# Performance work log

Measured on AMD Instinct MI355X. Metric: run time of the kernel, lower is better.

Reference implementation:

```python
import jax, jax.numpy as jnp
import numpy as np

B, N, E, F_IN, F_OUT = 4, 50000, 800000, 128, 128


def setup_inputs() -> dict:
    key = jax.random.key(0)
    k1, k2, k3, k4, k5 = jax.random.split(key, 5)
    x = jax.random.normal(k1, (B, N, F_IN), dtype=jnp.float32)
    # nn.Linear(in, out, bias=False) weight: [out_features, in_features]
    W = jax.random.normal(k2, (F_OUT, F_IN), dtype=jnp.float32) * (1.0 / np.sqrt(F_IN))
    edge_row = jax.random.randint(k3, (E,), 0, N, dtype=jnp.int64)
    edge_col = jax.random.randint(k4, (E,), 0, N, dtype=jnp.int64)
    edge_vals = jax.random.uniform(k5, (E,), dtype=jnp.float32)
    return {"x": x, "W": W, "edge_row": edge_row, "edge_col": edge_col, "edge_vals": edge_vals}


def reference(x, W, edge_row, edge_col, edge_vals):
    # x: [B, N, F_in]; linear projection (no bias): h = x @ W^T -> [B, N, F_out]
    h = jnp.einsum('bnf,of->bno', x, W)

    # SpMM: out[r] = sum_{edges (r,c)} A[r,c] * h[c], vmapped over batch
    def spmm(hb):  # hb: [N, F_out]
        msg = hb[edge_col] * edge_vals[:, None]  # [E, F_out]
        return jax.ops.segment_sum(msg, edge_row, num_segments=N)

    return jax.vmap(spmm)(h)  # [B, N, F_out]
```

## Files before the change

### kernel.cpp

```cpp
#include <hip/hip_runtime.h>
#include <stdint.h>

#define NB 4
#define NN 50000
#define NE 800000
#define NF 128

#define NBLK 49
#define LDW 136

typedef __attribute__((ext_vector_type(8))) short  bfrag;
typedef __attribute__((ext_vector_type(4))) float  ffrag;
typedef __attribute__((ext_vector_type(4))) short  short4v;
typedef __attribute__((ext_vector_type(4))) float  f32x4;

__device__ inline unsigned short f2bf(float f) {
    unsigned int u = __builtin_bit_cast(unsigned int, f);
    u += 0x7fffu + ((u >> 16) & 1u);
    return (unsigned short)(u >> 16);
}
__device__ inline float bflo(unsigned int u) { return __builtin_bit_cast(float, u << 16); }
__device__ inline float bfhi(unsigned int u) { return __builtin_bit_cast(float, u & 0xffff0000u); }

__global__ __launch_bounds__(256) void gemm_kernel(
    const float* __restrict__ x,
    const float* __restrict__ W,
    unsigned short* __restrict__ h,
    const int* __restrict__ erow,
    int* __restrict__ cnt,
    int M)
{
    __shared__ short wsh[128 * LDW];

    const int tid = threadIdx.x;

    for (int e = blockIdx.x * 256 + tid; e < NE; e += gridDim.x * 256)
        atomicAdd(&cnt[erow[e]], 1);

#pragma unroll
    for (int it = 0; it < 16; ++it) {
        int idx = it * 256 + tid;
        int r   = idx >> 5;
        int c4  = idx & 31;
        float4 wv = *(const float4*)(W + (size_t)r * NF + c4 * 4);
        short4v wsv;
        wsv[0] = (short)f2bf(wv.x); wsv[1] = (short)f2bf(wv.y);
        wsv[2] = (short)f2bf(wv.z); wsv[3] = (short)f2bf(wv.w);
        *(short4v*)&wsh[r * LDW + c4 * 4] = wsv;
    }
    __syncthreads();

    const int w    = tid >> 6;
    const int lane = tid & 63;
    const int q    = lane >> 4;
    const int l15  = lane & 15;
    const int r0   = blockIdx.x * 128 + w * 32;

    const float* xp[2];
#pragma unroll
    for (int i = 0; i < 2; ++i) {
        int gr = r0 + i * 16 + l15;
        gr = gr < M ? gr : M - 1;
        xp[i] = x + (size_t)gr * NF + q * 8;
    }

    ffrag acc[2][8];
#pragma unroll
    for (int i = 0; i < 2; ++i)
#pragma unroll
        for (int j = 0; j < 8; ++j) acc[i][j] = (ffrag)0.f;

#pragma unroll 2
    for (int kc = 0; kc < 4; ++kc) {
        bfrag a[2];
#pragma unroll
        for (int i = 0; i < 2; ++i) {
            float4 u0 = *(const float4*)(xp[i] + kc * 32);
            float4 u1 = *(const float4*)(xp[i] + kc * 32 + 4);
            bfrag t;
            t[0] = (short)f2bf(u0.x); t[1] = (short)f2bf(u0.y);
            t[2] = (short)f2bf(u0.z); t[3] = (short)f2bf(u0.w);
            t[4] = (short)f2bf(u1.x); t[5] = (short)f2bf(u1.y);
            t[6] = (short)f2bf(u1.z); t[7] = (short)f2bf(u1.w);
            a[i] = t;
        }
#pragma unroll
        for (int j = 0; j < 8; ++j) {
            bfrag b = *(const bfrag*)&wsh[(j * 16 + l15) * LDW + kc * 32 + q * 8];
            acc[0][j] = __builtin_amdgcn_mfma_f32_16x16x32_bf16(
                a[0], b, acc[0][j], 0, 0, 0);
            acc[1][j] = __builtin_amdgcn_mfma_f32_16x16x32_bf16(
                a[1], b, acc[1][j], 0, 0, 0);
        }
    }

    __syncthreads();
    short* tile = wsh;
#pragma unroll
    for (int i = 0; i < 2; ++i)
#pragma unroll
        for (int reg = 0; reg < 4; ++reg) {
            int row = w * 32 + i * 16 + q * 4 + reg;
#pragma unroll
            for (int j = 0; j < 8; ++j)
                tile[row * LDW + j * 16 + l15] = (short)f2bf(acc[i][j][reg]);
        }
    __syncthreads();
#pragma unroll
    for (int it = 0; it < 8; ++it) {
        int row = it * 16 + (tid >> 4);
        int m   = blockIdx.x * 128 + row;
        if (m < M) {
            int n  = m % NN;
            int bb = m / NN;
            uint4 v = *(const uint4*)&tile[row * LDW + (tid & 15) * 8];
            *(uint4*)(h + ((size_t)n * NB + bb) * NF + (tid & 15) * 8) = v;
        }
    }
}

__global__ __launch_bounds__(1024) void scan1_kernel(
    const int* __restrict__ cnt, int* __restrict__ rs, int* __restrict__ bsum)
{
    __shared__ int wsum[16];
    const int tid  = threadIdx.x;
    const int lane = tid & 63;
    const int wid  = tid >> 6;
    const int i    = blockIdx.x * 1024 + tid;

    int v = (i < NN) ? cnt[i] : 0;
    int incl = v;
#pragma unroll
    for (int off = 1; off < 64; off <<= 1) {
        int t = __shfl_up(incl, off, 64);
        if (lane >= off) incl += t;
    }
    if (lane == 63) wsum[wid] = incl;
    __syncthreads();
    int woff = 0;
    for (int ww = 0; ww < wid; ++ww) woff += wsum[ww];
    if (i < NN) rs[i] = woff + incl - v;
    if (tid == 0) {
        int tot = 0;
        for (int ww = 0; ww < 16; ++ww) tot += wsum[ww];
        bsum[blockIdx.x] = tot;
    }
}

__global__ void scan2_kernel(int* __restrict__ bsum)
{
    int lane = threadIdx.x;
    int v = (lane < NBLK) ? bsum[lane] : 0;
    int incl = v;
#pragma unroll
    for (int off = 1; off < 64; off <<= 1) {
        int t = __shfl_up(incl, off, 64);
        if (lane >= off) incl += t;
    }
    if (lane < NBLK) bsum[lane] = incl - v;
}

__global__ void scatter_kernel(const int* __restrict__ row,
                               const int* __restrict__ col,
                               const float* __restrict__ val,
                               const int* __restrict__ rs,
                               const int* __restrict__ bsum,
                               int* __restrict__ cursor,
                               uint2* __restrict__ cv_s)
{
    int e = blockIdx.x * 256 + threadIdx.x;
    if (e < NE) {
        int r   = row[e];
        int p   = atomicAdd(&cursor[r], 1);
        int dst = rs[r] + bsum[r >> 10] + p;
        uint2 cv;
        cv.x = (unsigned)col[e];
        cv.y = __builtin_bit_cast(unsigned, val[e]);
        cv_s[dst] = cv;
    }
}

__global__ __launch_bounds__(256) void spmm_kernel(
    const unsigned short* __restrict__ h,
    const int* __restrict__ rs,
    const int* __restrict__ bsum,
    const uint2* __restrict__ cv_s,
    float* __restrict__ out)
{
    const int w    = threadIdx.x >> 6;
    const int lane = threadIdx.x & 63;
    int r = blockIdx.x * 4 + w;
    if (r >= NN) return;
    r = __builtin_amdgcn_readfirstlane(r);

    const int s = rs[r] + bsum[r >> 10];
    const int e = (r + 1 == NN) ? NE : rs[r + 1] + bsum[(r + 1) >> 10];
    const int b    = lane >> 4;
    const int loff = b * NF + (lane & 15) * 8;

    float acc[8];
#pragma unroll
    for (int k = 0; k < 8; ++k) acc[k] = 0.f;

    for (int base = s; base < e; base += 64) {
        const int n = min(64, e - base);
        unsigned long long cvp = 0ull;
        if (lane < n)
            cvp = __builtin_nontemporal_load(
                      (const unsigned long long*)(cv_s + base + lane));
        const int cvx = (int)(unsigned)(cvp & 0xffffffffull);
        const int cvy = (int)(unsigned)(cvp >> 32);

        const int n4 = (n + 3) & ~3;
        for (int i = 0; i < n4; i += 4) {
            const unsigned c0 = (unsigned)__builtin_amdgcn_readlane(cvx, i);
            const unsigned c1 = (unsigned)__builtin_amdgcn_readlane(cvx, i + 1);
            const unsigned c2 = (unsigned)__builtin_amdgcn_readlane(cvx, i + 2);
            const unsigned c3 = (unsigned)__builtin_amdgcn_readlane(cvx, i + 3);
            const uint4 q0 = *(const uint4*)(h + (size_t)c0 * (NB * NF) + loff);
            const uint4 q1 = *(const uint4*)(h + (size_t)c1 * (NB * NF) + loff);
            const uint4 q2 = *(const uint4*)(h + (size_t)c2 * (NB * NF) + loff);
            const uint4 q3 = *(const uint4*)(h + (size_t)c3 * (NB * NF) + loff);
            const float v0 = __builtin_bit_cast(
                float, __builtin_amdgcn_readlane(cvy, i));
            const float v1 = __builtin_bit_cast(
                float, __builtin_amdgcn_readlane(cvy, i + 1));
            const float v2 = __builtin_bit_cast(
                float, __builtin_amdgcn_readlane(cvy, i + 2));
            const float v3 = __builtin_bit_cast(
                float, __builtin_amdgcn_readlane(cvy, i + 3));

            acc[0] += v0 * bflo(q0.x); acc[1] += v0 * bfhi(q0.x);
            acc[2] += v0 * bflo(q0.y); acc[3] += v0 * bfhi(q0.y);
            acc[4] += v0 * bflo(q0.z); acc[5] += v0 * bfhi(q0.z);
            acc[6] += v0 * bflo(q0.w); acc[7] += v0 * bfhi(q0.w);
            acc[0] += v1 * bflo(q1.x); acc[1] += v1 * bfhi(q1.x);
            acc[2] += v1 * bflo(q1.y); acc[3] += v1 * bfhi(q1.y);
            acc[4] += v1 * bflo(q1.z); acc[5] += v1 * bfhi(q1.z);
            acc[6] += v1 * bflo(q1.w); acc[7] += v1 * bfhi(q1.w);
            acc[0] += v2 * bflo(q2.x); acc[1] += v2 * bfhi(q2.x);
            acc[2] += v2 * bflo(q2.y); acc[3] += v2 * bfhi(q2.y);
            acc[4] += v2 * bflo(q2.z); acc[5] += v2 * bfhi(q2.z);
            acc[6] += v2 * bflo(q2.w); acc[7] += v2 * bfhi(q2.w);
            acc[0] += v3 * bflo(q3.x); acc[1] += v3 * bfhi(q3.x);
            acc[2] += v3 * bflo(q3.y); acc[3] += v3 * bfhi(q3.y);
            acc[4] += v3 * bflo(q3.z); acc[5] += v3 * bfhi(q3.z);
            acc[6] += v3 * bflo(q3.w); acc[7] += v3 * bfhi(q3.w);
        }
    }

    float* op = out + ((size_t)b * NN + r) * NF + (lane & 15) * 8;
    *(float4*)op       = make_float4(acc[0], acc[1], acc[2], acc[3]);
    *(float4*)(op + 4) = make_float4(acc[4], acc[5], acc[6], acc[7]);
}

extern "C" void kernel_launch(void* const* d_in, const int* in_sizes, int n_in,
                              void* d_out, int out_size, void* d_ws, size_t ws_size,
                              hipStream_t stream)
{
    const float* x    = (const float*)d_in[0];
    const float* W    = (const float*)d_in[1];
    const int*   erow = (const int*)d_in[2];
    const int*   ecol = (const int*)d_in[3];
    const float* ev   = (const float*)d_in[4];
    float*       out  = (float*)d_out;

    char*  ws  = (char*)d_ws;
    size_t off = 0;
    auto alloc = [&](size_t bytes) -> void* {
        void* p = ws + off;
        off += (bytes + 255) & ~(size_t)255;
        return p;
    };
    unsigned short* h = (unsigned short*)alloc((size_t)NN * NB * NF * sizeof(unsigned short));
    int*   rs     = (int*)  alloc((size_t)(NN + 1) * sizeof(int));
    int*   cnt    = (int*)  alloc((size_t)2 * NN * sizeof(int));
    int*   cursor = cnt + NN;
    int*   bsum   = (int*)  alloc((size_t)64 * sizeof(int));
    uint2* cv_s   = (uint2*)alloc((size_t)NE * sizeof(uint2));

    hipMemsetAsync(cnt, 0, (size_t)2 * NN * sizeof(int), stream);

    const int M = NB * NN;
    gemm_kernel<<<(M + 127) / 128, 256, 0, stream>>>(x, W, h, erow, cnt, M);

    scan1_kernel<<<NBLK, 1024, 0, stream>>>(cnt, rs, bsum);
    scan2_kernel<<<1, 64, 0, stream>>>(bsum);
    scatter_kernel<<<(NE + 255) / 256, 256, 0, stream>>>(erow, ecol, ev, rs,
                                                         bsum, cursor, cv_s);

    spmm_kernel<<<(NN + 3) / 4, 256, 0, stream>>>(h, rs, bsum, cv_s, out);
}
```

Measured before the change: 378.5 us.

## Merge two-level scan into one block, reuse counts as cursor, unroll gather by 8

Replaces the two-kernel block scan with a single 1024-thread block where each thread scans a chunk of 49 counts serially. The row-start array is now absolute, which drops the bsum indirection from scatter and spmm. Scatter decrements the count array in place instead of using a separate cursor, so the memset only clears half as much. The spmm gather loop is unrolled to 8 outstanding 16-byte loads per iteration to raise memory-level parallelism, at the cost of more registers and padded work on short rows. The single-block scan has strided, uncoalesced per-thread reads and runs on one CU.

Measured after the change: 463.6 us. +22.5%, slower.

```diff
diff --git a/kernel.cpp b/kernel.cpp
--- a/kernel.cpp
+++ b/kernel.cpp
@@ -6,13 +6,13 @@
 #define NE 800000
 #define NF 128
 
-#define NBLK 49
+#define SCHUNK 49
 #define LDW 136
 
 typedef __attribute__((ext_vector_type(8))) short  bfrag;
 typedef __attribute__((ext_vector_type(4))) float  ffrag;
 typedef __attribute__((ext_vector_type(4))) short  short4v;
-typedef __attribute__((ext_vector_type(4))) float  f32x4;
+typedef __attribute__((ext_vector_type(4))) unsigned int u32x4;
 
 __device__ inline unsigned short f2bf(float f) {
     unsigned int u = __builtin_bit_cast(unsigned int, f);
@@ -119,60 +119,51 @@
     }
 }
 
-__global__ __launch_bounds__(1024) void scan1_kernel(
-    const int* __restrict__ cnt, int* __restrict__ rs, int* __restrict__ bsum)
-{
-    __shared__ int wsum[16];
+__global__ __launch_bounds__(1024) void scan_kernel(
+    const int* __restrict__ cnt, int* __restrict__ rs)
+{
+    __shared__ int woffs[16];
     const int tid  = threadIdx.x;
     const int lane = tid & 63;
     const int wid  = tid >> 6;
-    const int i    = blockIdx.x * 1024 + tid;
-
-    int v = (i < NN) ? cnt[i] : 0;
-    int incl = v;
+    const int i0   = tid * SCHUNK;
+
+    int sum = 0;
+    for (int j = 0; j < SCHUNK; ++j) {
+        int i = i0 + j;
+        sum += (i < NN) ? cnt[i] : 0;
+    }
+    int incl = sum;
 #pragma unroll
     for (int off = 1; off < 64; off <<= 1) {
         int t = __shfl_up(incl, off, 64);
         if (lane >= off) incl += t;
     }
-    if (lane == 63) wsum[wid] = incl;
+    if (lane == 63) woffs[wid] = incl;
     __syncthreads();
     int woff = 0;
-    for (int ww = 0; ww < wid; ++ww) woff += wsum[ww];
-    if (i < NN) rs[i] = woff + incl - v;
-    if (tid == 0) {
-        int tot = 0;
-        for (int ww = 0; ww < 16; ++ww) tot += wsum[ww];
-        bsum[blockIdx.x] = tot;
-    }
-}
-
-__global__ void scan2_kernel(int* __restrict__ bsum)
-{
-    int lane = threadIdx.x;
-    int v = (lane < NBLK) ? bsum[lane] : 0;
-    int incl = v;
-#pragma unroll
-    for (int off = 1; off < 64; off <<= 1) {
-        int t = __shfl_up(incl, off, 64);
-        if (lane >= off) incl += t;
-    }
-    if (lane < NBLK) bsum[lane] = incl - v;
+    for (int ww = 0; ww < wid; ++ww) woff += woffs[ww];
+    int run = woff + incl - sum;
+
+    for (int j = 0; j < SCHUNK; ++j) {
+        int i = i0 + j;
+        if (i < NN) { rs[i] = run; run += cnt[i]; }
+    }
+    if (tid == 0) rs[NN] = NE;
 }
 
 __global__ void scatter_kernel(const int* __restrict__ row,
                                const int* __restrict__ col,
                                const float* __restrict__ val,
                                const int* __restrict__ rs,
-                               const int* __restrict__ bsum,
-                               int* __restrict__ cursor,
+                               int* __restrict__ cnt,
                                uint2* __restrict__ cv_s)
 {
     int e = blockIdx.x * 256 + threadIdx.x;
     if (e < NE) {
         int r   = row[e];
-        int p   = atomicAdd(&cursor[r], 1);
-        int dst = rs[r] + bsum[r >> 10] + p;
+        int p   = atomicSub(&cnt[r], 1) - 1;
+        int dst = rs[r] + p;
         uint2 cv;
         cv.x = (unsigned)col[e];
         cv.y = __builtin_bit_cast(unsigned, val[e]);
@@ -183,7 +174,6 @@
 __global__ __launch_bounds__(256) void spmm_kernel(
     const unsigned short* __restrict__ h,
     const int* __restrict__ rs,
-    const int* __restrict__ bsum,
     const uint2* __restrict__ cv_s,
     float* __restrict__ out)
 {
@@ -193,8 +183,8 @@
     if (r >= NN) return;
     r = __builtin_amdgcn_readfirstlane(r);
 
-    const int s = rs[r] + bsum[r >> 10];
-    const int e = (r + 1 == NN) ? NE : rs[r + 1] + bsum[(r + 1) >> 10];
+    const int s = rs[r];
+    const int e = rs[r + 1];
     const int b    = lane >> 4;
     const int loff = b * NF + (lane & 15) * 8;
 
@@ -211,41 +201,25 @@
         const int cvx = (int)(unsigned)(cvp & 0xffffffffull);
         const int cvy = (int)(unsigned)(cvp >> 32);
 
-        const int n4 = (n + 3) & ~3;
-        for (int i = 0; i < n4; i += 4) {
-            const unsigned c0 = (unsigned)__builtin_amdgcn_readlane(cvx, i);
-            const unsigned c1 = (unsigned)__builtin_amdgcn_readlane(cvx, i + 1);
-            const unsigned c2 = (unsigned)__builtin_amdgcn_readlane(cvx, i + 2);
-            const unsigned c3 = (unsigned)__builtin_amdgcn_readlane(cvx, i + 3);
-            const uint4 q0 = *(const uint4*)(h + (size_t)c0 * (NB * NF) + loff);
-            const uint4 q1 = *(const uint4*)(h + (size_t)c1 * (NB * NF) + loff);
-            const uint4 q2 = *(const uint4*)(h + (size_t)c2 * (NB * NF) + loff);
-            const uint4 q3 = *(const uint4*)(h + (size_t)c3 * (NB * NF) + loff);
-            const float v0 = __builtin_bit_cast(
-                float, __builtin_amdgcn_readlane(cvy, i));
-            const float v1 = __builtin_bit_cast(
-                float, __builtin_amdgcn_readlane(cvy, i + 1));
-            const float v2 = __builtin_bit_cast(
-                float, __builtin_amdgcn_readlane(cvy, i + 2));
-            const float v3 = __builtin_bit_cast(
-                float, __builtin_amdgcn_readlane(cvy, i + 3));
-
-            acc[0] += v0 * bflo(q0.x); acc[1] += v0 * bfhi(q0.x);
-            acc[2] += v0 * bflo(q0.y); acc[3] += v0 * bfhi(q0.y);
-            acc[4] += v0 * bflo(q0.z); acc[5] += v0 * bfhi(q0.z);
-            acc[6] += v0 * bflo(q0.w); acc[7] += v0 * bfhi(q0.w);
-            acc[0] += v1 * bflo(q1.x); acc[1] += v1 * bfhi(q1.x);
-            acc[2] += v1 * bflo(q1.y); acc[3] += v1 * bfhi(q1.y);
-            acc[4] += v1 * bflo(q1.z); acc[5] += v1 * bfhi(q1.z);
-            acc[6] += v1 * bflo(q1.w); acc[7] += v1 * bfhi(q1.w);
-            acc[0] += v2 * bflo(q2.x); acc[1] += v2 * bfhi(q2.x);
-            acc[2] += v2 * bflo(q2.y); acc[3] += v2 * bfhi(q2.y);
-            acc[4] += v2 * bflo(q2.z); acc[5] += v2 * bfhi(q2.z);
-            acc[6] += v2 * bflo(q2.w); acc[7] += v2 * bfhi(q2.w);
-            acc[0] += v3 * bflo(q3.x); acc[1] += v3 * bfhi(q3.x);
-            acc[2] += v3 * bflo(q3.y); acc[3] += v3 * bfhi(q3.y);
-            acc[4] += v3 * bflo(q3.z); acc[5] += v3 * bfhi(q3.z);
-            acc[6] += v3 * bflo(q3.w); acc[7] += v3 * bfhi(q3.w);
+        const int n8 = (n + 7) & ~7;
+        for (int i = 0; i < n8; i += 8) {
+            unsigned c[8];
+            u32x4 q[8];
+#pragma unroll
+            for (int k = 0; k < 8; ++k)
+                c[k] = (unsigned)__builtin_amdgcn_readlane(cvx, i + k);
+#pragma unroll
+            for (int k = 0; k < 8; ++k)
+                q[k] = *(const u32x4*)(h + (size_t)c[k] * (NB * NF) + loff);
+#pragma unroll
+            for (int k = 0; k < 8; ++k) {
+                const float v = __builtin_bit_cast(
+                    float, __builtin_amdgcn_readlane(cvy, i + k));
+                acc[0] += v * bflo(q[k][0]); acc[1] += v * bfhi(q[k][0]);
+                acc[2] += v * bflo(q[k][1]); acc[3] += v * bfhi(q[k][1]);
+                acc[4] += v * bflo(q[k][2]); acc[5] += v * bfhi(q[k][2]);
+                acc[6] += v * bflo(q[k][3]); acc[7] += v * bfhi(q[k][3]);
+            }
         }
     }
 
@@ -273,21 +247,18 @@
         return p;
     };
     unsigned short* h = (unsigned short*)alloc((size_t)NN * NB * NF * sizeof(unsigned short));
-    int*   rs     = (int*)  alloc((size_t)(NN + 1) * sizeof(int));
-    int*   cnt    = (int*)  alloc((size_t)2 * NN * sizeof(int));
-    int*   cursor = cnt + NN;
-    int*   bsum   = (int*)  alloc((size_t)64 * sizeof(int));
-    uint2* cv_s   = (uint2*)alloc((size_t)NE * sizeof(uint2));
-
-    hipMemsetAsync(cnt, 0, (size_t)2 * NN * sizeof(int), stream);
+    int*   rs   = (int*)  alloc((size_t)(NN + 1) * sizeof(int));
+    int*   cnt  = (int*)  alloc((size_t)NN * sizeof(int));
+    uint2* cv_s = (uint2*)alloc((size_t)NE * sizeof(uint2));
+
+    hipMemsetAsync(cnt, 0, (size_t)NN * sizeof(int), stream);
 
     const int M = NB * NN;
     gemm_kernel<<<(M + 127) / 128, 256, 0, stream>>>(x, W, h, erow, cnt, M);
 
-    scan1_kernel<<<NBLK, 1024, 0, stream>>>(cnt, rs, bsum);
-    scan2_kernel<<<1, 64, 0, stream>>>(bsum);
+    scan_kernel<<<1, 1024, 0, stream>>>(cnt, rs);
     scatter_kernel<<<(NE + 255) / 256, 256, 0, stream>>>(erow, ecol, ev, rs,
-                                                         bsum, cursor, cv_s);
-
-    spmm_kernel<<<(NN + 3) / 4, 256, 0, stream>>>(h, rs, bsum, cv_s, out);
-}
+                                                         cnt, cv_s);
+
+    spmm_kernel<<<(NN + 3) / 4, 256, 0, stream>>>(h, rs, cv_s, out);
+}
```

## Fuse gemm, scan and scatter into one cooperative persistent kernel

Applied to the files above, without the earlier changes.

Replaces the memset, gemm, two scan kernels and scatter with a single cooperative launch of 512 persistent blocks that use grid.sync between phases. The cnt array is now reused as the scatter cursor by decrementing it, which drops the separate cursor buffer and its memset. The scan uses 256-wide blocks with a two-level prefix. The point is to remove several kernel launches and their gaps. In exchange the GEMM runs as a grid-stride persistent loop that restages W for every tile, and grid-wide barriers add their own cost. A non-cooperative fallback path is kept.

New measurement: 593.8 us. +56.9%, slower.

```diff
diff --git a/kernel.cpp b/kernel.cpp
--- a/kernel.cpp
+++ b/kernel.cpp
@@ -1,18 +1,24 @@
 #include <hip/hip_runtime.h>
+#include <hip/hip_cooperative_groups.h>
 #include <stdint.h>
+
+namespace cg = cooperative_groups;
 
 #define NB 4
 #define NN 50000
 #define NE 800000
 #define NF 128
 
-#define NBLK 49
-#define LDW 136
+#define GRID  512
+#define NTHR  256
+#define GSTR  (GRID * NTHR)
+#define NTILE 1563
+#define NSBLK 196
+#define LDW   136
 
 typedef __attribute__((ext_vector_type(8))) short  bfrag;
 typedef __attribute__((ext_vector_type(4))) float  ffrag;
 typedef __attribute__((ext_vector_type(4))) short  short4v;
-typedef __attribute__((ext_vector_type(4))) float  f32x4;
 
 __device__ inline unsigned short f2bf(float f) {
     unsigned int u = __builtin_bit_cast(unsigned int, f);
@@ -22,21 +28,82 @@
 __device__ inline float bflo(unsigned int u) { return __builtin_bit_cast(float, u << 16); }
 __device__ inline float bfhi(unsigned int u) { return __builtin_bit_cast(float, u & 0xffff0000u); }
 
-__global__ __launch_bounds__(256) void gemm_kernel(
-    const float* __restrict__ x,
-    const float* __restrict__ W,
-    unsigned short* __restrict__ h,
-    const int* __restrict__ erow,
-    int* __restrict__ cnt,
-    int M)
-{
-    __shared__ short wsh[128 * LDW];
-
-    const int tid = threadIdx.x;
-
-    for (int e = blockIdx.x * 256 + tid; e < NE; e += gridDim.x * 256)
-        atomicAdd(&cnt[erow[e]], 1);
-
+__device__ __forceinline__ void gemm_tile(
+    const float* __restrict__ x, unsigned short* __restrict__ h,
+    short* wsh, int t, int M, int tid)
+{
+    const int w    = tid >> 6;
+    const int lane = tid & 63;
+    const int q    = lane >> 4;
+    const int l15  = lane & 15;
+    const int r0   = t * 128 + w * 32;
+
+    const float* xp[2];
+#pragma unroll
+    for (int i = 0; i < 2; ++i) {
+        int gr = r0 + i * 16 + l15;
+        gr = gr < M ? gr : M - 1;
+        xp[i] = x + (size_t)gr * NF + q * 8;
+    }
+
+    ffrag acc[2][8];
+#pragma unroll
+    for (int i = 0; i < 2; ++i)
+#pragma unroll
+        for (int j = 0; j < 8; ++j) acc[i][j] = (ffrag)0.f;
+
+#pragma unroll 2
+    for (int kc = 0; kc < 4; ++kc) {
+        bfrag a[2];
+#pragma unroll
+        for (int i = 0; i < 2; ++i) {
+            float4 u0 = *(const float4*)(xp[i] + kc * 32);
+            float4 u1 = *(const float4*)(xp[i] + kc * 32 + 4);
+            bfrag tt;
+            tt[0] = (short)f2bf(u0.x); tt[1] = (short)f2bf(u0.y);
+            tt[2] = (short)f2bf(u0.z); tt[3] = (short)f2bf(u0.w);
+            tt[4] = (short)f2bf(u1.x); tt[5] = (short)f2bf(u1.y);
+            tt[6] = (short)f2bf(u1.z); tt[7] = (short)f2bf(u1.w);
+            a[i] = tt;
+        }
+#pragma unroll
+        for (int j = 0; j < 8; ++j) {
+            bfrag b = *(const bfrag*)&wsh[(j * 16 + l15) * LDW + kc * 32 + q * 8];
+            acc[0][j] = __builtin_amdgcn_mfma_f32_16x16x32_bf16(
+                a[0], b, acc[0][j], 0, 0, 0);
+            acc[1][j] = __builtin_amdgcn_mfma_f32_16x16x32_bf16(
+                a[1], b, acc[1][j], 0, 0, 0);
+        }
+    }
+
+    __syncthreads();
+    short* tile = wsh;
+#pragma unroll
+    for (int i = 0; i < 2; ++i)
+#pragma unroll
+        for (int reg = 0; reg < 4; ++reg) {
+            int row = w * 32 + i * 16 + q * 4 + reg;
+#pragma unroll
+            for (int j = 0; j < 8; ++j)
+                tile[row * LDW + j * 16 + l15] = (short)f2bf(acc[i][j][reg]);
+        }
+    __syncthreads();
+#pragma unroll
+    for (int it = 0; it < 8; ++it) {
+        int row = it * 16 + (tid >> 4);
+        int m   = t * 128 + row;
+        if (m < M) {
+            int n  = m % NN;
+            int bb = m / NN;
+            uint4 v = *(const uint4*)&tile[row * LDW + (tid & 15) * 8];
+            *(uint4*)(h + ((size_t)n * NB + bb) * NF + (tid & 15) * 8) = v;
+        }
+    }
+}
+
+__device__ __forceinline__ void stage_W(const float* __restrict__ W,
+                                        short* wsh, int tid)
+{
 #pragma unroll
     for (int it = 0; it < 16; ++it) {
         int idx = it * 256 + tid;
@@ -48,86 +115,111 @@
         wsv[2] = (short)f2bf(wv.z); wsv[3] = (short)f2bf(wv.w);
         *(short4v*)&wsh[r * LDW + c4 * 4] = wsv;
     }
-    __syncthreads();
-
+}
+
+__global__ __launch_bounds__(256, 2) void front_kernel(
+    const float* __restrict__ x,
+    const float* __restrict__ W,
+    unsigned short* __restrict__ h,
+    const int* __restrict__ erow,
+    const int* __restrict__ ecol,
+    const float* __restrict__ ev,
+    int* __restrict__ rs,
+    int* __restrict__ cnt,
+    int* __restrict__ bsum,
+    uint2* __restrict__ cv_s)
+{
+    __shared__ short wsh[128 * LDW];
+    int* iw = (int*)wsh;
+
+    const int tid  = threadIdx.x;
+    const int gid  = blockIdx.x * NTHR + tid;
     const int w    = tid >> 6;
     const int lane = tid & 63;
-    const int q    = lane >> 4;
-    const int l15  = lane & 15;
-    const int r0   = blockIdx.x * 128 + w * 32;
-
-    const float* xp[2];
-#pragma unroll
-    for (int i = 0; i < 2; ++i) {
-        int gr = r0 + i * 16 + l15;
-        gr = gr < M ? gr : M - 1;
-        xp[i] = x + (size_t)gr * NF + q * 8;
-    }
-
-    ffrag acc[2][8];
-#pragma unroll
-    for (int i = 0; i < 2; ++i)
-#pragma unroll
-        for (int j = 0; j < 8; ++j) acc[i][j] = (ffrag)0.f;
-
-#pragma unroll 2
-    for (int kc = 0; kc < 4; ++kc) {
-        bfrag a[2];
-#pragma unroll
-        for (int i = 0; i < 2; ++i) {
-            float4 u0 = *(const float4*)(xp[i] + kc * 32);
-            float4 u1 = *(const float4*)(xp[i] + kc * 32 + 4);
-            bfrag t;
-            t[0] = (short)f2bf(u0.x); t[1] = (short)f2bf(u0.y);
-            t[2] = (short)f2bf(u0.z); t[3] = (short)f2bf(u0.w);
-            t[4] = (short)f2bf(u1.x); t[5] = (short)f2bf(u1.y);
-            t[6] = (short)f2bf(u1.z); t[7] = (short)f2bf(u1.w);
-            a[i] = t;
-        }
-#pragma unroll
-        for (int j = 0; j < 8; ++j) {
-            bfrag b = *(const bfrag*)&wsh[(j * 16 + l15) * LDW + kc * 32 + q * 8];
-            acc[0][j] = __builtin_amdgcn_mfma_f32_16x16x32_bf16(
-                a[0], b, acc[0][j], 0, 0, 0);
-            acc[1][j] = __builtin_amdgcn_mfma_f32_16x16x32_bf16(
-                a[1], b, acc[1][j], 0, 0, 0);
-        }
-    }
-
-    __syncthreads();
-    short* tile = wsh;
-#pragma unroll
-    for (int i = 0; i < 2; ++i)
-#pragma unroll
-        for (int reg = 0; reg < 4; ++reg) {
-            int row = w * 32 + i * 16 + q * 4 + reg;
-#pragma unroll
-            for (int j = 0; j < 8; ++j)
-                tile[row * LDW + j * 16 + l15] = (short)f2bf(acc[i][j][reg]);
-        }
-    __syncthreads();
-#pragma unroll
-    for (int it = 0; it < 8; ++it) {
-        int row = it * 16 + (tid >> 4);
-        int m   = blockIdx.x * 128 + row;
-        if (m < M) {
-            int n  = m % NN;
-            int bb = m / NN;
-            uint4 v = *(const uint4*)&tile[row * LDW + (tid & 15) * 8];
-            *(uint4*)(h + ((size_t)n * NB + bb) * NF + (tid & 15) * 8) = v;
-        }
-    }
-}
-
-__global__ __launch_bounds__(1024) void scan1_kernel(
+    const int M    = NB * NN;
+    cg::grid_group grid = cg::this_grid();
+
+    for (int i = gid; i < NN; i += GSTR) cnt[i] = 0;
+    grid.sync();
+
+    for (int e = gid; e < NE; e += GSTR)
+        atomicAdd(&cnt[erow[e]], 1);
+
+    for (int t = blockIdx.x; t < NTILE; t += GRID) {
+        __syncthreads();
+        stage_W(W, wsh, tid);
+        __syncthreads();
+        gemm_tile(x, h, wsh, t, M, tid);
+    }
+    grid.sync();
+
+    if (blockIdx.x < NSBLK) {
+        int i = blockIdx.x * 256 + tid;
+        int v = (i < NN) ? cnt[i] : 0;
+        int incl = v;
+#pragma unroll
+        for (int off = 1; off < 64; off <<= 1) {
+            int tshf = __shfl_up(incl, off, 64);
+            if (lane >= off) incl += tshf;
+        }
+        if (lane == 63) iw[w] = incl;
+        __syncthreads();
+        int woff = 0;
+        for (int ww = 0; ww < w; ++ww) woff += iw[ww];
+        if (i < NN) rs[i] = woff + incl - v;
+        if (tid == 255) bsum[blockIdx.x] = woff + incl;
+    }
+    grid.sync();
+
+    if (blockIdx.x == 0) {
+        int v = (tid < NSBLK) ? bsum[tid] : 0;
+        int incl = v;
+#pragma unroll
+        for (int off = 1; off < 64; off <<= 1) {
+            int tshf = __shfl_up(incl, off, 64);
+            if (lane >= off) incl += tshf;
+        }
+        if (lane == 63) iw[w] = incl;
+        __syncthreads();
+        int woff = 0;
+        for (int ww = 0; ww < w; ++ww) woff += iw[ww];
+        if (tid < NSBLK) bsum[tid] = woff + incl - v;
+    }
+    grid.sync();
+
+    for (int e = gid; e < NE; e += GSTR) {
+        int r   = erow[e];
+        int p   = atomicSub(&cnt[r], 1) - 1;
+        int dst = rs[r] + bsum[r >> 8] + p;
+        uint2 cv;
+        cv.x = (unsigned)ecol[e];
+        cv.y = __builtin_bit_cast(unsigned, ev[e]);
+        cv_s[dst] = cv;
+    }
+}
+
+__global__ __launch_bounds__(256) void gemm_fb(
+    const float* __restrict__ x, const float* __restrict__ W,
+    unsigned short* __restrict__ h, const int* __restrict__ erow,
+    int* __restrict__ cnt, int M)
+{
+    __shared__ short wsh[128 * LDW];
+    const int tid = threadIdx.x;
+    for (int e = blockIdx.x * 256 + tid; e < NE; e += gridDim.x * 256)
+        atomicAdd(&cnt[erow[e]], 1);
+    stage_W(W, wsh, tid);
+    __syncthreads();
+    gemm_tile(x, h, wsh, blockIdx.x, M, tid);
+}
+
+__global__ __launch_bounds__(256) void scan1_fb(
     const int* __restrict__ cnt, int* __restrict__ rs, int* __restrict__ bsum)
 {
-    __shared__ int wsum[16];
+    __shared__ int iw[4];
     const int tid  = threadIdx.x;
     const int lane = tid & 63;
-    const int wid  = tid >> 6;
-    const int i    = blockIdx.x * 1024 + tid;
-
+    const int w    = tid >> 6;
+    int i = blockIdx.x * 256 + tid;
     int v = (i < NN) ? cnt[i] : 0;
     int incl = v;
 #pragma unroll
@@ -135,44 +227,47 @@
         int t = __shfl_up(incl, off, 64);
         if (lane >= off) incl += t;
     }
-    if (lane == 63) wsum[wid] = incl;
+    if (lane == 63) iw[w] = incl;
     __syncthreads();
     int woff = 0;
-    for (int ww = 0; ww < wid; ++ww) woff += wsum[ww];
+    for (int ww = 0; ww < w; ++ww) woff += iw[ww];
     if (i < NN) rs[i] = woff + incl - v;
-    if (tid == 0) {
-        int tot = 0;
-        for (int ww = 0; ww < 16; ++ww) tot += wsum[ww];
-        bsum[blockIdx.x] = tot;
-    }
-}
-
-__global__ void scan2_kernel(int* __restrict__ bsum)
-{
-    int lane = threadIdx.x;
-    int v = (lane < NBLK) ? bsum[lane] : 0;
+    if (tid == 255) bsum[blockIdx.x] = woff + incl;
+}
+
+__global__ __launch_bounds__(256) void scan2_fb(int* __restrict__ bsum)
+{
+    __shared__ int iw[4];
+    const int tid  = threadIdx.x;
+    const int lane = tid & 63;
+    const int w    = tid >> 6;
+    int v = (tid < NSBLK) ? bsum[tid] : 0;
     int incl = v;
 #pragma unroll
     for (int off = 1; off < 64; off <<= 1) {
         int t = __shfl_up(incl, off, 64);
         if (lane >= off) incl += t;
     }
-    if (lane < NBLK) bsum[lane] = incl - v;
-}
-
-__global__ void scatter_kernel(const int* __restrict__ row,
-                               const int* __restrict__ col,
-                               const float* __restrict__ val,
-                               const int* __restrict__ rs,
-                               const int* __restrict__ bsum,
-                               int* __restrict__ cursor,
-                               uint2* __restrict__ cv_s)
+    if (lane == 63) iw[w] = incl;
+    __syncthreads();
+    int woff = 0;
+    for (int ww = 0; ww < w; ++ww) woff += iw[ww];
+    if (tid < NSBLK) bsum[tid] = woff + incl - v;
+}
+
+__global__ void scatter_fb(const int* __restrict__ row,
+                           const int* __restrict__ col,
+                           const float* __restrict__ val,
+                           const int* __restrict__ rs,
+                           const int* __restrict__ bsum,
+                           int* __restrict__ cnt,
+                           uint2* __restrict__ cv_s)
 {
     int e = blockIdx.x * 256 + threadIdx.x;
     if (e < NE) {
         int r   = row[e];
-        int p   = atomicAdd(&cursor[r], 1);
-        int dst = rs[r] + bsum[r >> 10] + p;
+        int p   = atomicSub(&cnt[r], 1) - 1;
+        int dst = rs[r] + bsum[r >> 8] + p;
         uint2 cv;
         cv.x = (unsigned)col[e];
         cv.y = __builtin_bit_cast(unsigned, val[e]);
@@ -193,8 +288,8 @@
     if (r >= NN) return;
     r = __builtin_amdgcn_readfirstlane(r);
 
-    const int s = rs[r] + bsum[r >> 10];
-    const int e = (r + 1 == NN) ? NE : rs[r + 1] + bsum[(r + 1) >> 10];
+    const int s = rs[r] + bsum[r >> 8];
+    const int e = (r + 1 == NN) ? NE : rs[r + 1] + bsum[(r + 1) >> 8];
     const int b    = lane >> 4;
     const int loff = b * NF + (lane & 15) * 8;
 
@@ -273,21 +368,25 @@
         return p;
     };
     unsigned short* h = (unsigned short*)alloc((size_t)NN * NB * NF * sizeof(unsigned short));
-    int*   rs     = (int*)  alloc((size_t)(NN + 1) * sizeof(int));
-    int*   cnt    = (int*)  alloc((size_t)2 * NN * sizeof(int));
-    int*   cursor = cnt + NN;
-    int*   bsum   = (int*)  alloc((size_t)64 * sizeof(int));
-    uint2* cv_s   = (uint2*)alloc((size_t)NE * sizeof(uint2));
-
-    hipMemsetAsync(cnt, 0, (size_t)2 * NN * sizeof(int), stream);
+    int*   rs   = (int*)  alloc((size_t)(NN + 1) * sizeof(int));
+    int*   cnt  = (int*)  alloc((size_t)NN * sizeof(int));
+    int*   bsum = (int*)  alloc((size_t)256 * sizeof(int));
+    uint2* cv_s = (uint2*)alloc((size_t)NE * sizeof(uint2));
 
     const int M = NB * NN;
-    gemm_kernel<<<(M + 127) / 128, 256, 0, stream>>>(x, W, h, erow, cnt, M);
-
-    scan1_kernel<<<NBLK, 1024, 0, stream>>>(cnt, rs, bsum);
-    scan2_kernel<<<1, 64, 0, stream>>>(bsum);
-    scatter_kernel<<<(NE + 255) / 256, 256, 0, stream>>>(erow, ecol, ev, rs,
-                                                         bsum, cursor, cv_s);
+
+    void* args[] = {(void*)&x, (void*)&W, (void*)&h, (void*)&erow, (void*)&ecol,
+                    (void*)&ev, (void*)&rs, (void*)&cnt, (void*)&bsum, (void*)&cv_s};
+    hipError_t cerr = hipLaunchCooperativeKernel((void*)front_kernel, dim3(GRID),
+                                                 dim3(NTHR), args, 0, stream);
+    if (cerr != hipSuccess) {
+        hipMemsetAsync(cnt, 0, (size_t)NN * sizeof(int), stream);
+        gemm_fb<<<NTILE, 256, 0, stream>>>(x, W, h, erow, cnt, M);
+        scan1_fb<<<NSBLK, 256, 0, stream>>>(cnt, rs, bsum);
+        scan2_fb<<<1, 256, 0, stream>>>(bsum);
+        scatter_fb<<<(NE + 255) / 256, 256, 0, stream>>>(erow, ecol, ev, rs,
+                                                         bsum, cnt, cv_s);
+    }
 
     spmm_kernel<<<(NN + 3) / 4, 256, 0, stream>>>(h, rs, bsum, cv_s, out);
 }
```

## Shard edge-count atomics across eight copies and precompute per-copy scatter cursors

Applied to the files above, without the earlier changes.

Row-degree counting now spreads atomics over eight strided copies of the count array, keyed by edge index, which cuts contention on hot rows. A third scan kernel folds the block offsets into rs and turns the per-copy counts into running end cursors. Scatter then uses atomicSub on those cursors to get final positions directly, so it no longer reads rs or bsum. This adds an extra kernel launch and eight times the count memory to zero, scan and read, while spmm reads rs without the bsum correction.

New measurement: 386.2 us. 2.0% more time.

```diff
diff --git a/kernel.cpp b/kernel.cpp
--- a/kernel.cpp
+++ b/kernel.cpp
@@ -6,13 +6,15 @@
 #define NE 800000
 #define NF 128
 
-#define NBLK 49
-#define LDW 136
+#define NSBLK 196
+#define NNP   50176
+#define NCPY  8
+#define NTILE 1563
+#define LDW   136
 
 typedef __attribute__((ext_vector_type(8))) short  bfrag;
 typedef __attribute__((ext_vector_type(4))) float  ffrag;
 typedef __attribute__((ext_vector_type(4))) short  short4v;
-typedef __attribute__((ext_vector_type(4))) float  f32x4;
 
 __device__ inline unsigned short f2bf(float f) {
     unsigned int u = __builtin_bit_cast(unsigned int, f);
@@ -27,7 +29,7 @@
     const float* __restrict__ W,
     unsigned short* __restrict__ h,
     const int* __restrict__ erow,
-    int* __restrict__ cnt,
+    int* __restrict__ cnt8,
     int M)
 {
     __shared__ short wsh[128 * LDW];
@@ -35,7 +37,7 @@
     const int tid = threadIdx.x;
 
     for (int e = blockIdx.x * 256 + tid; e < NE; e += gridDim.x * 256)
-        atomicAdd(&cnt[erow[e]], 1);
+        atomicAdd(&cnt8[(e & 7) * NNP + erow[e]], 1);
 
 #pragma unroll
     for (int it = 0; it < 16; ++it) {
@@ -77,12 +79,12 @@
         for (int i = 0; i < 2; ++i) {
             float4 u0 = *(const float4*)(xp[i] + kc * 32);
             float4 u1 = *(const float4*)(xp[i] + kc * 32 + 4);
-            bfrag t;
-            t[0] = (short)f2bf(u0.x); t[1] = (short)f2bf(u0.y);
-            t[2] = (short)f2bf(u0.z); t[3] = (short)f2bf(u0.w);
-            t[4] = (short)f2bf(u1.x); t[5] = (short)f2bf(u1.y);
-            t[6] = (short)f2bf(u1.z); t[7] = (short)f2bf(u1.w);
-            a[i] = t;
+            bfrag tt;
+            tt[0] = (short)f2bf(u0.x); tt[1] = (short)f2bf(u0.y);
+            tt[2] = (short)f2bf(u0.z); tt[3] = (short)f2bf(u0.w);
+            tt[4] = (short)f2bf(u1.x); tt[5] = (short)f2bf(u1.y);
+            tt[6] = (short)f2bf(u1.z); tt[7] = (short)f2bf(u1.w);
+            a[i] = tt;
         }
 #pragma unroll
         for (int j = 0; j < 8; ++j) {
@@ -119,71 +121,90 @@
     }
 }
 
-__global__ __launch_bounds__(1024) void scan1_kernel(
-    const int* __restrict__ cnt, int* __restrict__ rs, int* __restrict__ bsum)
-{
-    __shared__ int wsum[16];
+__global__ __launch_bounds__(256) void scan1_kernel(
+    const int* __restrict__ cnt8, int* __restrict__ rs, int* __restrict__ bsum)
+{
+    __shared__ int iw[4];
     const int tid  = threadIdx.x;
     const int lane = tid & 63;
-    const int wid  = tid >> 6;
-    const int i    = blockIdx.x * 1024 + tid;
-
-    int v = (i < NN) ? cnt[i] : 0;
+    const int w    = tid >> 6;
+    const int i    = blockIdx.x * 256 + tid;
+
+    int v = 0;
+    if (i < NN)
+#pragma unroll
+        for (int c = 0; c < NCPY; ++c) v += cnt8[c * NNP + i];
+
     int incl = v;
 #pragma unroll
     for (int off = 1; off < 64; off <<= 1) {
         int t = __shfl_up(incl, off, 64);
         if (lane >= off) incl += t;
     }
-    if (lane == 63) wsum[wid] = incl;
+    if (lane == 63) iw[w] = incl;
     __syncthreads();
     int woff = 0;
-    for (int ww = 0; ww < wid; ++ww) woff += wsum[ww];
+    for (int ww = 0; ww < w; ++ww) woff += iw[ww];
     if (i < NN) rs[i] = woff + incl - v;
-    if (tid == 0) {
-        int tot = 0;
-        for (int ww = 0; ww < 16; ++ww) tot += wsum[ww];
-        bsum[blockIdx.x] = tot;
-    }
-}
-
-__global__ void scan2_kernel(int* __restrict__ bsum)
-{
-    int lane = threadIdx.x;
-    int v = (lane < NBLK) ? bsum[lane] : 0;
+    if (tid == 255) bsum[blockIdx.x] = woff + incl;
+}
+
+__global__ __launch_bounds__(256) void scan2_kernel(int* __restrict__ bsum)
+{
+    __shared__ int iw[4];
+    const int tid  = threadIdx.x;
+    const int lane = tid & 63;
+    const int w    = tid >> 6;
+    int v = (tid < NSBLK) ? bsum[tid] : 0;
     int incl = v;
 #pragma unroll
     for (int off = 1; off < 64; off <<= 1) {
         int t = __shfl_up(incl, off, 64);
         if (lane >= off) incl += t;
     }
-    if (lane < NBLK) bsum[lane] = incl - v;
+    if (lane == 63) iw[w] = incl;
+    __syncthreads();
+    int woff = 0;
+    for (int ww = 0; ww < w; ++ww) woff += iw[ww];
+    if (tid < NSBLK) bsum[tid] = woff + incl - v;
+}
+
+__global__ __launch_bounds__(256) void scan3_kernel(
+    int* __restrict__ rs, const int* __restrict__ bsum, int* __restrict__ cnt8)
+{
+    const int i = blockIdx.x * 256 + threadIdx.x;
+    if (i < NN) {
+        int run = rs[i] + bsum[i >> 8];
+        rs[i] = run;
+#pragma unroll
+        for (int c = 0; c < NCPY; ++c) {
+            run += cnt8[c * NNP + i];
+            cnt8[c * NNP + i] = run;
+        }
+    }
+    if (i == 0) rs[NN] = NE;
 }
 
 __global__ void scatter_kernel(const int* __restrict__ row,
                                const int* __restrict__ col,
                                const float* __restrict__ val,
-                               const int* __restrict__ rs,
-                               const int* __restrict__ bsum,
-                               int* __restrict__ cursor,
+                               int* __restrict__ cur8,
                                uint2* __restrict__ cv_s)
 {
     int e = blockIdx.x * 256 + threadIdx.x;
     if (e < NE) {
-        int r   = row[e];
-        int p   = atomicAdd(&cursor[r], 1);
-        int dst = rs[r] + bsum[r >> 10] + p;
+        int r = row[e];
+        int p = atomicSub(&cur8[(e & 7) * NNP + r], 1) - 1;
         uint2 cv;
         cv.x = (unsigned)col[e];
         cv.y = __builtin_bit_cast(unsigned, val[e]);
-        cv_s[dst] = cv;
+        cv_s[p] = cv;
     }
 }
 
 __global__ __launch_bounds__(256) void spmm_kernel(
     const unsigned short* __restrict__ h,
     const int* __restrict__ rs,
-    const int* __restrict__ bsum,
     const uint2* __restrict__ cv_s,
     float* __restrict__ out)
 {
@@ -193,8 +214,8 @@
     if (r >= NN) return;
     r = __builtin_amdgcn_readfirstlane(r);
 
-    const int s = rs[r] + bsum[r >> 10];
-    const int e = (r + 1 == NN) ? NE : rs[r + 1] + bsum[(r + 1) >> 10];
+    const int s = rs[r];
+    const int e = rs[r + 1];
     const int b    = lane >> 4;
     const int loff = b * NF + (lane & 15) * 8;
 
@@ -273,21 +294,21 @@
         return p;
     };
     unsigned short* h = (unsigned short*)alloc((size_t)NN * NB * NF * sizeof(unsigned short));
-    int*   rs     = (int*)  alloc((size_t)(NN + 1) * sizeof(int));
-    int*   cnt    = (int*)  alloc((size_t)2 * NN * sizeof(int));
-    int*   cursor = cnt + NN;
-    int*   bsum   = (int*)  alloc((size_t)64 * sizeof(int));
-    uint2* cv_s   = (uint2*)alloc((size_t)NE * sizeof(uint2));
-
-    hipMemsetAsync(cnt, 0, (size_t)2 * NN * sizeof(int), stream);
+    int*   rs   = (int*)  alloc((size_t)(NN + 1) * sizeof(int));
+    int*   cnt8 = (int*)  alloc((size_t)NCPY * NNP * sizeof(int));
+    int*   bsum = (int*)  alloc((size_t)256 * sizeof(int));
+    uint2* cv_s = (uint2*)alloc((size_t)NE * sizeof(uint2));
+
+    hipMemsetAsync(cnt8, 0, (size_t)NCPY * NNP * sizeof(int), stream);
 
     const int M = NB * NN;
-    gemm_kernel<<<(M + 127) / 128, 256, 0, stream>>>(x, W, h, erow, cnt, M);
-
-    scan1_kernel<<<NBLK, 1024, 0, stream>>>(cnt, rs, bsum);
-    scan2_kernel<<<1, 64, 0, stream>>>(bsum);
-    scatter_kernel<<<(NE + 255) / 256, 256, 0, stream>>>(erow, ecol, ev, rs,
-                                                         bsum, cursor, cv_s);
-
-    spmm_kernel<<<(NN + 3) / 4, 256, 0, stream>>>(h, rs, bsum, cv_s, out);
-}
+    gemm_kernel<<<NTILE, 256, 0, stream>>>(x, W, h, erow, cnt8, M);
+
+    scan1_kernel<<<NSBLK, 256, 0, stream>>>(cnt8, rs, bsum);
+    scan2_kernel<<<1, 256, 0, stream>>>(bsum);
+    scan3_kernel<<<NSBLK, 256, 0, stream>>>(rs, bsum, cnt8);
+    scatter_kernel<<<(NE + 255) / 256, 256, 0, stream>>>(erow, ecol, ev,
+                                                         cnt8, cv_s);
+
+    spmm_kernel<<<(NN + 3) / 4, 256, 0, stream>>>(h, rs, cv_s, out);
+}
```
